# Kernel optimization log

Hardware: AMD Instinct MI355X
Metric: run time of the kernel (lower is better)

## Reference

```python
import jax, jax.numpy as jnp
import numpy as np
import jax.scipy.linalg as jsl

K = 4           # num_hops + 1
N = 4096        # nodes
D = 256         # in_dim == out_dim
S = 32          # subspace_dim
ETA = 0.5
EPS = 0.5


def setup_inputs() -> dict:
    key = jax.random.key(0)
    k1, k2, k3 = jax.random.split(key, 3)
    hops = jax.random.normal(k1, (K, N, D), dtype=jnp.float32)
    A = (jax.random.uniform(k2, (N, N)) < 0.01).astype(jnp.float32)
    A = jnp.maximum(A, A.T)
    A = jnp.fill_diagonal(A, 1.0, inplace=False)
    deg = A.sum(axis=1)
    L = jnp.diag(deg) - A  # graph Laplacian
    # orthonormal subspace bases via QR, as in __init__
    raw = jax.random.normal(k3, (K, D, S), dtype=jnp.float32)
    q, _ = jnp.linalg.qr(raw)
    U = q[:, :, :S]
    hop_weights = jnp.ones((K,), dtype=jnp.float32) / K
    threshold = jnp.full((D,), 0.05, dtype=jnp.float32)
    lambda_lap = jnp.asarray(0.1, dtype=jnp.float32)
    return {"hops": hops, "adj_mask": A, "L": L, "U": U,
            "hop_weights": hop_weights, "threshold": threshold,
            "lambda_lap": lambda_lap}


def reference(hops, adj_mask, L, U, hop_weights, threshold, lambda_lap):
    n = hops.shape[1]
    s = U.shape[-1]
    w = jax.nn.softmax(hop_weights, axis=0)
    mask_add = (1.0 - adj_mask) * -1e9  # [n, n]
    I_s = jnp.eye(s, dtype=hops.dtype)
    agg_total = jnp.zeros((hops.shape[2], n), dtype=hops.dtype)  # [d, n]
    coeff = s / (n * EPS ** 2)
    for k in range(K):  # small fixed hop count
        Uk = U[k]                      # [d, s]
        Zk = Uk.T @ hops[k].T          # [s, n]
        M_k = I_s + coeff * (Zk @ Zk.T)  # [s, s]
        cf = jsl.cho_factor(M_k)
        M_inv = jsl.cho_solve(cf, I_s)   # Cholesky inverse
        MZ = M_inv @ Zk                  # [s, n]
        scores = Zk.T @ MZ + mask_add    # [n, n] Mahalanobis-style attention
        alpha = jax.nn.softmax(scores, axis=1)
        grad_k = Uk @ (MZ @ alpha.T)     # [d, n]
        agg_total = agg_total + w[k] * grad_k
    H_agg = agg_total.T                  # [n, d]
    lap_grad = lambda_lap * (L @ H_agg)
    H_half = hops[0] + ETA * H_agg - ETA * lap_grad
    # soft-threshold (proximal step); in_dim == out_dim so no proj
    H_out = jnp.sign(H_half) * jax.nn.relu(jnp.abs(H_half) - threshold[None, :])
    # orthogonality regularizer over subspace bases
    orth_loss = jnp.asarray(0.0, dtype=hops.dtype)
    for k in range(K):
        UkTUk = U[k].T @ U[k]
        orth_loss = orth_loss + ((UkTUk - I_s) ** 2).sum()
        for l in range(k + 1, K):
            orth_loss = orth_loss + ((U[k].T @ U[l]) ** 2).sum()
    lap_smooth = jnp.sum(H_out * (L @ H_out))  # trace(H^T L H)
    return (H_out, orth_loss, lap_smooth, jax.lax.stop_gradient(w))
```

## Files before the change

kernel.cpp:

```cpp
#include <hip/hip_runtime.h>
#include <cstddef>

typedef unsigned short ushortt;
typedef unsigned int uintt;

static constexpr int Nn = 4096;
static constexpr int Dd = 256;
static constexpr int Ss = 32;
static constexpr int Kk = 4;
static constexpr int CAP = 160;
static constexpr float kEta   = 0.5f;
static constexpr float kCoeff = 0.03125f;

__device__ __forceinline__ float waveReduceSum(float v){
  #pragma unroll
  for (int off = 32; off > 0; off >>= 1) v += __shfl_down(v, off, 64);
  return v;
}
__device__ __forceinline__ float blo(uintt u){ return __uint_as_float(u << 16); }
__device__ __forceinline__ float bhi(uintt u){ return __uint_as_float(u & 0xffff0000u); }
__device__ __forceinline__ ushortt f2b(float x){
  uintt u = __float_as_uint(x);
  uintt r = (u + 0x7fffu + ((u >> 16) & 1u)) >> 16;
  return (ushortt)r;
}
__device__ __forceinline__ float b2f(ushortt u){ return __uint_as_float(((uintt)u) << 16); }

__global__ __launch_bounds__(256) void build_kernel(const float* __restrict__ A,
                                                    const float* __restrict__ hw,
                                                    int* __restrict__ deg,
                                                    int* __restrict__ colx,
                                                    float* __restrict__ out){
  int i = blockIdx.x, tid = threadIdx.x;
  if (i == 0 && tid == 0){
    out[1048576] = 0.f;
    out[1048577] = 0.f;
    float a0=hw[0], a1=hw[1], a2=hw[2], a3=hw[3];
    float mx = fmaxf(fmaxf(a0,a1), fmaxf(a2,a3));
    float e0=expf(a0-mx), e1=expf(a1-mx), e2=expf(a2-mx), e3=expf(a3-mx);
    float s = e0+e1+e2+e3;
    out[1048578]=e0/s; out[1048579]=e1/s; out[1048580]=e2/s; out[1048581]=e3/s;
  }
  int lane = tid & 63, w = tid >> 6;
  __shared__ int wbuf[4][96];
  __shared__ int wcnt[4];
  const float4* row4 = (const float4*)(A + (size_t)i * Nn);
  int cnt = 0;
  int base = w * 256;
  #pragma unroll
  for (int it = 0; it < 4; it++){
    int c4 = base + it * 64 + lane;
    float4 v = row4[c4];
    int f0 = (v.x != 0.f), f1 = (v.y != 0.f), f2 = (v.z != 0.f), f3 = (v.w != 0.f);
    int nf = f0 + f1 + f2 + f3;
    int pre = nf;
    #pragma unroll
    for (int off = 1; off < 64; off <<= 1){
      int o = __shfl_up(pre, off, 64);
      if (lane >= off) pre += o;
    }
    int tot = __shfl(pre, 63, 64);
    int pos = cnt + pre - nf;
    int j0 = c4 * 4;
    if (f0){ if (pos < 96) wbuf[w][pos] = j0;     pos++; }
    if (f1){ if (pos < 96) wbuf[w][pos] = j0 + 1; pos++; }
    if (f2){ if (pos < 96) wbuf[w][pos] = j0 + 2; pos++; }
    if (f3){ if (pos < 96) wbuf[w][pos] = j0 + 3; pos++; }
    cnt += tot;
  }
  if (cnt > 96) cnt = 96;
  if (lane == 0) wcnt[w] = cnt;
  __syncthreads();
  int off = 0;
  for (int ww = 0; ww < w; ww++) off += wcnt[ww];
  int total = wcnt[0] + wcnt[1] + wcnt[2] + wcnt[3];
  for (int idx = lane; idx < cnt; idx += 64){
    int p = off + idx;
    if (p < CAP) colx[(size_t)i * CAP + p] = wbuf[w][idx];
  }
  if (tid == 0) deg[i] = (total < CAP) ? total : CAP;
}

__global__ __launch_bounds__(256) void z_kernel(const float* __restrict__ hops,
                                                const float* __restrict__ U,
                                                float* __restrict__ Zt4){
  int b = blockIdx.x;
  int k = b >> 9;
  int i0 = (b & 511) * 8;
  __shared__ float Us[Ss][260];
  for (int t = threadIdx.x; t < Dd * Ss; t += 256){
    int s = t & 31, d = t >> 5;
    Us[s][d] = U[(size_t)k * Dd * Ss + t];
  }
  __syncthreads();
  int s = threadIdx.x & 31, ii = threadIdx.x >> 5;
  int i = i0 + ii;
  const float4* h4 = (const float4*)(hops + ((size_t)k * Nn + i) * Dd);
  const float4* u4 = (const float4*)(&Us[s][0]);
  float acc = 0.f;
  #pragma unroll 8
  for (int dq = 0; dq < 64; dq++){
    float4 h = h4[dq];
    float4 u = u4[dq];
    acc += h.x*u.x + h.y*u.y + h.z*u.z + h.w*u.w;
  }
  Zt4[(size_t)i * 128 + k * 32 + s] = acc;
}

__global__ __launch_bounds__(256) void mpart_kernel(const float* __restrict__ Zt4,
                                                    float* __restrict__ Mpart){
  int b = blockIdx.x;
  int k = b >> 4, ch = b & 15;
  int i0 = ch * 256;
  __shared__ float zs[256][33];
  for (int t = threadIdx.x; t < 256 * 32; t += 256){
    int ii = t >> 5, s = t & 31;
    zs[ii][s] = Zt4[(size_t)(i0 + ii) * 128 + k * 32 + s];
  }
  __syncthreads();
  int tid = threadIdx.x;
  int s2 = tid & 31, s1b = tid >> 5;
  float a0=0.f, a1=0.f, a2=0.f, a3=0.f;
  for (int ii = 0; ii < 256; ii++){
    float zc = zs[ii][s2];
    a0 = fmaf(zs[ii][s1b],      zc, a0);
    a1 = fmaf(zs[ii][8 + s1b],  zc, a1);
    a2 = fmaf(zs[ii][16 + s1b], zc, a2);
    a3 = fmaf(zs[ii][24 + s1b], zc, a3);
  }
  float* outp = Mpart + (size_t)b * 1024;
  outp[0 * 256 + tid] = a0;
  outp[1 * 256 + tid] = a1;
  outp[2 * 256 + tid] = a2;
  outp[3 * 256 + tid] = a3;
}

__global__ __launch_bounds__(256) void inv_kernel(const float* __restrict__ Mpart,
                                                  float* __restrict__ Minv){
  __shared__ float Msh[4][32][33];
  int tid = threadIdx.x;
  for (int e = tid; e < 4096; e += 256){
    int k = e >> 10, rc = e & 1023;
    float s = 0.f;
    for (int ch = 0; ch < 16; ch++) s += Mpart[(size_t)(k * 16 + ch) * 1024 + rc];
    int r = rc >> 5, c = rc & 31;
    Msh[k][r][c] = kCoeff * s + ((r == c) ? 1.f : 0.f);
  }
  __syncthreads();
  int k = tid >> 6, lane = tid & 63, r = lane & 31, half = lane >> 5;
  float a[32];
  #pragma unroll
  for (int j = 0; j < 32; j++) a[j] = half ? ((r == j) ? 1.f : 0.f) : Msh[k][r][j];
  #pragma unroll
  for (int p = 0; p < 32; p++){
    float app = __shfl(a[p], p, 64);
    float pinv = 1.f / app;
    float f = __shfl(a[p], r, 64);
    #pragma unroll
    for (int j = 0; j < 32; j++){
      float pr = __shfl(a[j], p + (half << 5), 64) * pinv;
      a[j] = (r == p) ? pr : fmaf(-f, pr, a[j]);
    }
  }
  if (half){
    #pragma unroll
    for (int j = 0; j < 32; j++) Minv[(size_t)k * 1024 + r * 32 + j] = a[j];
  }
}

__global__ __launch_bounds__(256) void mz_kernel(const float* __restrict__ Zt4,
                                                 const float* __restrict__ Minv,
                                                 ushortt* __restrict__ MZb){
  int b = blockIdx.x;
  int k = b >> 7;
  int i0 = (b & 127) * 32;
  __shared__ float mi[32][33];
  __shared__ float zs[32][33];
  for (int t = threadIdx.x; t < 1024; t += 256){
    int ii = t >> 5, s2 = t & 31;
    mi[ii][s2] = Minv[(size_t)k * 1024 + t];
    zs[ii][s2] = Zt4[(size_t)(i0 + ii) * 128 + k * 32 + s2];
  }
  __syncthreads();
  int s = threadIdx.x & 31;
  for (int rr = 0; rr < 4; rr++){
    int ii = rr * 8 + (threadIdx.x >> 5);
    float acc = 0.f;
    #pragma unroll
    for (int s2 = 0; s2 < 32; s2++) acc = fmaf(mi[s][s2], zs[ii][s2], acc);
    MZb[(size_t)(i0 + ii) * 128 + k * 32 + s] = f2b(acc);
  }
}

__global__ __launch_bounds__(256) void agg_kernel(const float* __restrict__ Zt4,
                                                  const ushortt* __restrict__ MZb,
                                                  const float* __restrict__ wvec,
                                                  const int* __restrict__ deg,
                                                  const int* __restrict__ colx,
                                                  float* __restrict__ Vw){
  int i = blockIdx.x, tid = threadIdx.x;
  int lane = tid & 63, k = tid >> 6;
  __shared__ int cols[CAP];
  __shared__ __align__(16) float zi[128];
  __shared__ float sc[4][CAP + 8];
  int m = deg[i];
  if (tid < 128) zi[tid] = Zt4[(size_t)i * 128 + tid];
  for (int t = tid; t < m; t += 256) cols[t] = colx[(size_t)i * CAP + t];
  __syncthreads();

  float zr[32];
  {
    const float4* z4 = (const float4*)(&zi[k * 32]);
    #pragma unroll
    for (int q = 0; q < 8; q++){
      float4 z = z4[q];
      zr[q*4+0]=z.x; zr[q*4+1]=z.y; zr[q*4+2]=z.z; zr[q*4+3]=z.w;
    }
  }
  float lmax = -3.0e38f;
  for (int t = lane; t < m; t += 64){
    int j = cols[t];
    const uint4* rp = (const uint4*)(MZb + ((size_t)j * 128 + k * 32));
    uint4 q0 = rp[0], q1 = rp[1], q2 = rp[2], q3 = rp[3];
    float acc = 0.f;
    acc += blo(q0.x)*zr[0] + bhi(q0.x)*zr[1] + blo(q0.y)*zr[2] + bhi(q0.y)*zr[3];
    acc += blo(q0.z)*zr[4] + bhi(q0.z)*zr[5] + blo(q0.w)*zr[6] + bhi(q0.w)*zr[7];
    acc += blo(q1.x)*zr[8] + bhi(q1.x)*zr[9] + blo(q1.y)*zr[10]+ bhi(q1.y)*zr[11];
    acc += blo(q1.z)*zr[12]+ bhi(q1.z)*zr[13]+ blo(q1.w)*zr[14]+ bhi(q1.w)*zr[15];
    acc += blo(q2.x)*zr[16]+ bhi(q2.x)*zr[17]+ blo(q2.y)*zr[18]+ bhi(q2.y)*zr[19];
    acc += blo(q2.z)*zr[20]+ bhi(q2.z)*zr[21]+ blo(q2.w)*zr[22]+ bhi(q2.w)*zr[23];
    acc += blo(q3.x)*zr[24]+ bhi(q3.x)*zr[25]+ blo(q3.y)*zr[26]+ bhi(q3.y)*zr[27];
    acc += blo(q3.z)*zr[28]+ bhi(q3.z)*zr[29]+ blo(q3.w)*zr[30]+ bhi(q3.w)*zr[31];
    sc[k][t] = acc;
    lmax = fmaxf(lmax, acc);
  }
  #pragma unroll
  for (int off = 32; off > 0; off >>= 1) lmax = fmaxf(lmax, __shfl_xor(lmax, off, 64));
  float lsum = 0.f;
  for (int t = lane; t < m; t += 64){
    float e = __expf(sc[k][t] - lmax);
    sc[k][t] = e;
    lsum += e;
  }
  #pragma unroll
  for (int off = 32; off > 0; off >>= 1) lsum += __shfl_xor(lsum, off, 64);
  float scale = wvec[k] / lsum;

  int c2 = lane & 15, h = lane >> 4;
  float a0 = 0.f, a1 = 0.f;
  #pragma unroll 4
  for (int t = h; t < m; t += 4){
    int j = cols[t];
    uintt u = *(const uintt*)(MZb + ((size_t)j * 128 + k * 32 + c2 * 2));
    float e = sc[k][t];
    a0 = fmaf(blo(u), e, a0);
    a1 = fmaf(bhi(u), e, a1);
  }
  a0 += __shfl_xor(a0, 16, 64); a0 += __shfl_xor(a0, 32, 64);
  a1 += __shfl_xor(a1, 16, 64); a1 += __shfl_xor(a1, 32, 64);
  if (h == 0){
    float2 v2 = make_float2(a0 * scale, a1 * scale);
    *(float2*)(Vw + (size_t)i * 128 + k * 32 + c2 * 2) = v2;
  }
}

__global__ __launch_bounds__(256) void gatherv_kernel(const float* __restrict__ Vw,
                                                      const float* __restrict__ lam_ptr,
                                                      const int* __restrict__ deg,
                                                      const int* __restrict__ colx,
                                                      float* __restrict__ cVc){
  int i = blockIdx.x, tid = threadIdx.x;
  int c = tid & 127, g = tid >> 7;
  __shared__ int cols[CAP];
  __shared__ float vred[2][128];
  int m = deg[i];
  for (int t = tid; t < m; t += 256) cols[t] = colx[(size_t)i * CAP + t];
  __syncthreads();
  float acc = 0.f;
  #pragma unroll 8
  for (int t = g; t < m; t += 2)
    acc += Vw[(size_t)cols[t] * 128 + c];
  vred[g][c] = acc;
  __syncthreads();
  if (tid < 128){
    float nb = vred[0][tid] + vred[1][tid];
    float lam = lam_ptr[0];
    float self = Vw[(size_t)i * 128 + tid];
    cVc[(size_t)i * 128 + tid] = kEta * (1.f - lam * (float)m) * self + kEta * lam * nb;
  }
}

__global__ __launch_bounds__(256) void transu_kernel(const float* __restrict__ U,
                                                     float* __restrict__ Ubt){
  int idx = blockIdx.x * 256 + threadIdx.x;
  int c = idx >> 8, d = idx & 255;
  int k = c >> 5, s = c & 31;
  Ubt[idx] = U[(size_t)k * Dd * Ss + (size_t)d * Ss + s];
}

__global__ __launch_bounds__(256) void houtblend_kernel(const float* __restrict__ cVc,
                                                        const float* __restrict__ Ubt,
                                                        const float* __restrict__ hops0,
                                                        const float* __restrict__ thr,
                                                        float* __restrict__ out,
                                                        ushortt* __restrict__ Hb){
  int i0 = blockIdx.x * 16;
  int tid = threadIdx.x;
  __shared__ float Cs[16][132];
  for (int t = tid; t < 16 * 128; t += 256){
    int ii = t >> 7, c = t & 127;
    Cs[ii][c] = cVc[(size_t)(i0 + ii) * 128 + c];
  }
  __syncthreads();
  int d4 = tid & 63, g = tid >> 6;
  float4 acc[4];
  #pragma unroll
  for (int r = 0; r < 4; r++) acc[r] = make_float4(0.f, 0.f, 0.f, 0.f);
  #pragma unroll 2
  for (int c = 0; c < 128; c++){
    float4 ub = ((const float4*)(Ubt + (size_t)c * 256))[d4];
    #pragma unroll
    for (int r = 0; r < 4; r++){
      float cs = Cs[g * 4 + r][c];
      acc[r].x = fmaf(cs, ub.x, acc[r].x);
      acc[r].y = fmaf(cs, ub.y, acc[r].y);
      acc[r].z = fmaf(cs, ub.z, acc[r].z);
      acc[r].w = fmaf(cs, ub.w, acc[r].w);
    }
  }
  float4 th = ((const float4*)thr)[d4];
  #pragma unroll
  for (int r = 0; r < 4; r++){
    int i = i0 + g * 4 + r;
    float4 hp = ((const float4*)(hops0 + (size_t)i * 256))[d4];
    float hx = hp.x + acc[r].x, hy = hp.y + acc[r].y;
    float hz = hp.z + acc[r].z, hw = hp.w + acc[r].w;
    float4 o;
    o.x = copysignf(fmaxf(fabsf(hx) - th.x, 0.f), hx);
    o.y = copysignf(fmaxf(fabsf(hy) - th.y, 0.f), hy);
    o.z = copysignf(fmaxf(fabsf(hz) - th.z, 0.f), hz);
    o.w = copysignf(fmaxf(fabsf(hw) - th.w, 0.f), hw);
    ((float4*)(out + (size_t)i * 256))[d4] = o;
    ushort4 hb;
    hb.x = f2b(o.x); hb.y = f2b(o.y); hb.z = f2b(o.z); hb.w = f2b(o.w);
    *((ushort4*)(Hb + (size_t)i * 256 + d4 * 4)) = hb;
  }
}

__global__ __launch_bounds__(256) void lap_kernel(const float* __restrict__ Hout,
                                                  const ushortt* __restrict__ Hb,
                                                  const int* __restrict__ deg,
                                                  const int* __restrict__ colx,
                                                  float* __restrict__ lap_part){
  int b = blockIdx.x;
  int i = b >> 1, half = b & 1;
  int tid = threadIdx.x;
  int dl = tid & 127, g = tid >> 7;
  int d = half * 128 + dl;
  __shared__ int cols[CAP];
  int m = deg[i];
  for (int t = tid; t < m; t += 256) cols[t] = colx[(size_t)i * CAP + t];
  __syncthreads();
  float nb = 0.f;
  #pragma unroll 8
  for (int t = g; t < m; t += 2)
    nb += b2f(Hb[(size_t)cols[t] * 256 + d]);
  float hi = Hout[(size_t)i * 256 + d];
  float part = -hi * nb;
  if (g == 0) part = fmaf((float)m * hi, hi, part);
  part = waveReduceSum(part);
  __shared__ float red[4];
  if ((tid & 63) == 0) red[tid >> 6] = part;
  __syncthreads();
  if (tid == 0) lap_part[b] = red[0] + red[1] + red[2] + red[3];
}

__global__ __launch_bounds__(256) void lapred_kernel(const float* __restrict__ lap_part,
                                                     float* __restrict__ out){
  int tid = threadIdx.x;
  float s = 0.f;
  const float4* p4 = (const float4*)lap_part;
  #pragma unroll
  for (int q = 0; q < 8; q++){
    float4 v = p4[q * 256 + tid];
    s += v.x + v.y + v.z + v.w;
  }
  s = waveReduceSum(s);
  __shared__ float red[4];
  if ((tid & 63) == 0) red[tid >> 6] = s;
  __syncthreads();
  if (tid == 0) out[1048577] = red[0] + red[1] + red[2] + red[3];
}

__global__ __launch_bounds__(256) void orth_kernel(const float* __restrict__ U,
                                                   float* __restrict__ orth_out){
  int g = blockIdx.x * 256 + threadIdx.x;
  int pair = g >> 10;
  int idx = g & 1023;
  int s1 = idx >> 5, s2 = idx & 31;
  const int pk_[10] = {0,0,0,0,1,1,1,2,2,3};
  const int pl_[10] = {0,1,2,3,1,2,3,2,3,3};
  int pk = pk_[pair], pl = pl_[pair];
  const float* Uk = U + (size_t)pk * Dd * Ss;
  const float* Ul = U + (size_t)pl * Dd * Ss;
  float dot = 0.f;
  for (int d = 0; d < Dd; d++) dot += Uk[d * Ss + s1] * Ul[d * Ss + s2];
  float val = dot - ((pk == pl && s1 == s2) ? 1.f : 0.f);
  val *= val;
  val = waveReduceSum(val);
  __shared__ float red[4];
  if ((threadIdx.x & 63) == 0) red[threadIdx.x >> 6] = val;
  __syncthreads();
  if (threadIdx.x == 0) atomicAdd(orth_out, red[0] + red[1] + red[2] + red[3]);
}

extern "C" void kernel_launch(void* const* d_in, const int* in_sizes, int n_in,
                              void* d_out, int out_size, void* d_ws, size_t ws_size,
                              hipStream_t stream)
{
  const float* hops = (const float*)d_in[0];
  const float* A    = (const float*)d_in[1];
  const float* L    = (const float*)d_in[2];
  const float* U    = (const float*)d_in[3];
  const float* hw   = (const float*)d_in[4];
  const float* thr  = (const float*)d_in[5];
  const float* lam  = (const float*)d_in[6];
  (void)L; (void)in_sizes; (void)n_in; (void)out_size; (void)ws_size;

  float* out = (float*)d_out;
  float* ws  = (float*)d_ws;

  float*   Zt4   = ws;
  float*   Vw    = ws + 524288;
  float*   cVc   = ws + 1048576;
  ushortt* MZb   = (ushortt*)(ws + 1572864);
  ushortt* Hb    = (ushortt*)(ws + 1835008);
  float*   Ubt   = ws + 2359296;
  float*   Mpart = ws + 2392064;
  float*   Minv  = ws + 2457600;
  int*     deg   = (int*)(ws + 2461696);
  int*     colx  = (int*)(ws + 2465792);
  float*   lapp  = ws + 3121152;

  float* orth_out = out + 1048576;
  float* w_out    = out + 1048578;

  build_kernel    <<<Nn, 256, 0, stream>>>(A, hw, deg, colx, out);
  transu_kernel   <<<128, 256, 0, stream>>>(U, Ubt);
  z_kernel        <<<Kk*512, 256, 0, stream>>>(hops, U, Zt4);
  mpart_kernel    <<<Kk*16, 256, 0, stream>>>(Zt4, Mpart);
  inv_kernel      <<<1, 256, 0, stream>>>(Mpart, Minv);
  mz_kernel       <<<Kk*128, 256, 0, stream>>>(Zt4, Minv, MZb);
  agg_kernel      <<<Nn, 256, 0, stream>>>(Zt4, MZb, w_out, deg, colx, Vw);
  gatherv_kernel  <<<Nn, 256, 0, stream>>>(Vw, lam, deg, colx, cVc);
  houtblend_kernel<<<256, 256, 0, stream>>>(cVc, Ubt, hops, thr, out, Hb);
  lap_kernel      <<<2*Nn, 256, 0, stream>>>(out, Hb, deg, colx, lapp);
  lapred_kernel   <<<1, 256, 0, stream>>>(lapp, out);
  orth_kernel     <<<40, 256, 0, stream>>>(U, orth_out);
}
```

Before: 317.8 us.

## Fuse neighbor gather into output blend and merge small kernels to cut launches

Folds the gatherv kernel into the output-blend kernel so each block gathers neighbor Vw rows itself and builds the blended coefficients in shared memory. This removes the cVc intermediate and one launch. The U transpose moves into z_kernel, the lap reduction becomes an extra block of orth_kernel, and agg_kernel's final gather now uses wider 8-byte loads with 4 accumulators. Together this drops three launches, but the fused kernel runs only 256 blocks for the gather work that previously used 4096 blocks, so occupancy and latency hiding may suffer.

New measurement: 329.6 us. +3.7%, slower.

```diff
diff --git a/kernel.cpp b/kernel.cpp
--- a/kernel.cpp
+++ b/kernel.cpp
@@ -83,7 +83,8 @@
 
 __global__ __launch_bounds__(256) void z_kernel(const float* __restrict__ hops,
                                                 const float* __restrict__ U,
-                                                float* __restrict__ Zt4){
+                                                float* __restrict__ Zt4,
+                                                float* __restrict__ Ubt){
   int b = blockIdx.x;
   int k = b >> 9;
   int i0 = (b & 511) * 8;
@@ -105,6 +106,12 @@
     acc += h.x*u.x + h.y*u.y + h.z*u.z + h.w*u.w;
   }
   Zt4[(size_t)i * 128 + k * 32 + s] = acc;
+  if (b < 128){
+    int idx = b * 256 + threadIdx.x;
+    int c = idx >> 8, d = idx & 255;
+    int kk = c >> 5, s2 = c & 31;
+    Ubt[idx] = U[(size_t)kk * Dd * Ss + (size_t)d * Ss + s2];
+  }
 }
 
 __global__ __launch_bounds__(256) void mpart_kernel(const float* __restrict__ Zt4,
@@ -246,70 +253,80 @@
   for (int off = 32; off > 0; off >>= 1) lsum += __shfl_xor(lsum, off, 64);
   float scale = wvec[k] / lsum;
 
-  int c2 = lane & 15, h = lane >> 4;
-  float a0 = 0.f, a1 = 0.f;
-  #pragma unroll 4
-  for (int t = h; t < m; t += 4){
+  int c8 = lane & 7, h = lane >> 3;
+  float a0 = 0.f, a1 = 0.f, a2 = 0.f, a3 = 0.f;
+  #pragma unroll 2
+  for (int t = h; t < m; t += 8){
     int j = cols[t];
-    uintt u = *(const uintt*)(MZb + ((size_t)j * 128 + k * 32 + c2 * 2));
+    uint2 u = *(const uint2*)(MZb + ((size_t)j * 128 + k * 32 + c8 * 4));
     float e = sc[k][t];
-    a0 = fmaf(blo(u), e, a0);
-    a1 = fmaf(bhi(u), e, a1);
-  }
-  a0 += __shfl_xor(a0, 16, 64); a0 += __shfl_xor(a0, 32, 64);
-  a1 += __shfl_xor(a1, 16, 64); a1 += __shfl_xor(a1, 32, 64);
+    a0 = fmaf(blo(u.x), e, a0);
+    a1 = fmaf(bhi(u.x), e, a1);
+    a2 = fmaf(blo(u.y), e, a2);
+    a3 = fmaf(bhi(u.y), e, a3);
+  }
+  #pragma unroll
+  for (int off = 8; off < 64; off <<= 1){
+    a0 += __shfl_xor(a0, off, 64);
+    a1 += __shfl_xor(a1, off, 64);
+    a2 += __shfl_xor(a2, off, 64);
+    a3 += __shfl_xor(a3, off, 64);
+  }
   if (h == 0){
-    float2 v2 = make_float2(a0 * scale, a1 * scale);
-    *(float2*)(Vw + (size_t)i * 128 + k * 32 + c2 * 2) = v2;
-  }
-}
-
-__global__ __launch_bounds__(256) void gatherv_kernel(const float* __restrict__ Vw,
-                                                      const float* __restrict__ lam_ptr,
-                                                      const int* __restrict__ deg,
-                                                      const int* __restrict__ colx,
-                                                      float* __restrict__ cVc){
-  int i = blockIdx.x, tid = threadIdx.x;
-  int c = tid & 127, g = tid >> 7;
-  __shared__ int cols[CAP];
-  __shared__ float vred[2][128];
-  int m = deg[i];
-  for (int t = tid; t < m; t += 256) cols[t] = colx[(size_t)i * CAP + t];
-  __syncthreads();
-  float acc = 0.f;
-  #pragma unroll 8
-  for (int t = g; t < m; t += 2)
-    acc += Vw[(size_t)cols[t] * 128 + c];
-  vred[g][c] = acc;
-  __syncthreads();
-  if (tid < 128){
-    float nb = vred[0][tid] + vred[1][tid];
-    float lam = lam_ptr[0];
-    float self = Vw[(size_t)i * 128 + tid];
-    cVc[(size_t)i * 128 + tid] = kEta * (1.f - lam * (float)m) * self + kEta * lam * nb;
-  }
-}
-
-__global__ __launch_bounds__(256) void transu_kernel(const float* __restrict__ U,
-                                                     float* __restrict__ Ubt){
-  int idx = blockIdx.x * 256 + threadIdx.x;
-  int c = idx >> 8, d = idx & 255;
-  int k = c >> 5, s = c & 31;
-  Ubt[idx] = U[(size_t)k * Dd * Ss + (size_t)d * Ss + s];
-}
-
-__global__ __launch_bounds__(256) void houtblend_kernel(const float* __restrict__ cVc,
+    float4 v4 = make_float4(a0 * scale, a1 * scale, a2 * scale, a3 * scale);
+    *(float4*)(Vw + (size_t)i * 128 + k * 32 + c8 * 4) = v4;
+  }
+}
+
+__global__ __launch_bounds__(256) void houtfused_kernel(const float* __restrict__ Vw,
                                                         const float* __restrict__ Ubt,
                                                         const float* __restrict__ hops0,
                                                         const float* __restrict__ thr,
+                                                        const float* __restrict__ lam_ptr,
+                                                        const int* __restrict__ deg,
+                                                        const int* __restrict__ colx,
                                                         float* __restrict__ out,
                                                         ushortt* __restrict__ Hb){
   int i0 = blockIdx.x * 16;
   int tid = threadIdx.x;
+  int lane = tid & 63, w = tid >> 6;
   __shared__ float Cs[16][132];
-  for (int t = tid; t < 16 * 128; t += 256){
-    int ii = t >> 7, c = t & 127;
-    Cs[ii][c] = cVc[(size_t)(i0 + ii) * 128 + c];
+  __shared__ int cols_s[16][CAP];
+  __shared__ int deg_s[16];
+  for (int rr = w; rr < 16; rr += 4){
+    int i = i0 + rr;
+    int m = deg[i];
+    if (lane == 0) deg_s[rr] = m;
+    for (int t = lane; t < m; t += 64) cols_s[rr][t] = colx[(size_t)i * CAP + t];
+  }
+  __syncthreads();
+  float lam = lam_ptr[0];
+  int nb2 = lane >> 5;
+  int c32 = lane & 31;
+  for (int rr = w; rr < 16; rr += 4){
+    int i = i0 + rr;
+    int m = deg_s[rr];
+    float4 acc = make_float4(0.f, 0.f, 0.f, 0.f);
+    for (int t = nb2; t < m; t += 2){
+      int j = cols_s[rr][t];
+      float4 v = ((const float4*)(Vw + (size_t)j * 128))[c32];
+      acc.x += v.x; acc.y += v.y; acc.z += v.z; acc.w += v.w;
+    }
+    acc.x += __shfl_xor(acc.x, 32, 64);
+    acc.y += __shfl_xor(acc.y, 32, 64);
+    acc.z += __shfl_xor(acc.z, 32, 64);
+    acc.w += __shfl_xor(acc.w, 32, 64);
+    if (nb2 == 0){
+      float4 self = ((const float4*)(Vw + (size_t)i * 128))[c32];
+      float ca = kEta * (1.f - lam * (float)m);
+      float cb = kEta * lam;
+      float4 o;
+      o.x = fmaf(ca, self.x, cb * acc.x);
+      o.y = fmaf(ca, self.y, cb * acc.y);
+      o.z = fmaf(ca, self.z, cb * acc.z);
+      o.w = fmaf(ca, self.w, cb * acc.w);
+      *(float4*)(&Cs[rr][c32 * 4]) = o;
+    }
   }
   __syncthreads();
   int d4 = tid & 63, g = tid >> 6;
@@ -375,26 +392,26 @@
   if (tid == 0) lap_part[b] = red[0] + red[1] + red[2] + red[3];
 }
 
-__global__ __launch_bounds__(256) void lapred_kernel(const float* __restrict__ lap_part,
-                                                     float* __restrict__ out){
+__global__ __launch_bounds__(256) void orth_kernel(const float* __restrict__ U,
+                                                   const float* __restrict__ lap_part,
+                                                   float* __restrict__ out){
   int tid = threadIdx.x;
-  float s = 0.f;
-  const float4* p4 = (const float4*)lap_part;
-  #pragma unroll
-  for (int q = 0; q < 8; q++){
-    float4 v = p4[q * 256 + tid];
-    s += v.x + v.y + v.z + v.w;
-  }
-  s = waveReduceSum(s);
-  __shared__ float red[4];
-  if ((tid & 63) == 0) red[tid >> 6] = s;
-  __syncthreads();
-  if (tid == 0) out[1048577] = red[0] + red[1] + red[2] + red[3];
-}
-
-__global__ __launch_bounds__(256) void orth_kernel(const float* __restrict__ U,
-                                                   float* __restrict__ orth_out){
-  int g = blockIdx.x * 256 + threadIdx.x;
+  if (blockIdx.x == 40){
+    float s = 0.f;
+    const float4* p4 = (const float4*)lap_part;
+    #pragma unroll
+    for (int q = 0; q < 8; q++){
+      float4 v = p4[q * 256 + tid];
+      s += v.x + v.y + v.z + v.w;
+    }
+    s = waveReduceSum(s);
+    __shared__ float redl[4];
+    if ((tid & 63) == 0) redl[tid >> 6] = s;
+    __syncthreads();
+    if (tid == 0) out[1048577] = redl[0] + redl[1] + redl[2] + redl[3];
+    return;
+  }
+  int g = blockIdx.x * 256 + tid;
   int pair = g >> 10;
   int idx = g & 1023;
   int s1 = idx >> 5, s2 = idx & 31;
@@ -409,9 +426,9 @@
   val *= val;
   val = waveReduceSum(val);
   __shared__ float red[4];
-  if ((threadIdx.x & 63) == 0) red[threadIdx.x >> 6] = val;
-  __syncthreads();
-  if (threadIdx.x == 0) atomicAdd(orth_out, red[0] + red[1] + red[2] + red[3]);
+  if ((tid & 63) == 0) red[tid >> 6] = val;
+  __syncthreads();
+  if (tid == 0) atomicAdd(out + 1048576, red[0] + red[1] + red[2] + red[3]);
 }
 
 extern "C" void kernel_launch(void* const* d_in, const int* in_sizes, int n_in,
@@ -432,7 +449,6 @@
 
   float*   Zt4   = ws;
   float*   Vw    = ws + 524288;
-  float*   cVc   = ws + 1048576;
   ushortt* MZb   = (ushortt*)(ws + 1572864);
   ushortt* Hb    = (ushortt*)(ws + 1835008);
   float*   Ubt   = ws + 2359296;
@@ -442,19 +458,15 @@
   int*     colx  = (int*)(ws + 2465792);
   float*   lapp  = ws + 3121152;
 
-  float* orth_out = out + 1048576;
-  float* w_out    = out + 1048578;
+  float* w_out = out + 1048578;
 
   build_kernel    <<<Nn, 256, 0, stream>>>(A, hw, deg, colx, out);
-  transu_kernel   <<<128, 256, 0, stream>>>(U, Ubt);
-  z_kernel        <<<Kk*512, 256, 0, stream>>>(hops, U, Zt4);
+  z_kernel        <<<Kk*512, 256, 0, stream>>>(hops, U, Zt4, Ubt);
   mpart_kernel    <<<Kk*16, 256, 0, stream>>>(Zt4, Mpart);
   inv_kernel      <<<1, 256, 0, stream>>>(Mpart, Minv);
   mz_kernel       <<<Kk*128, 256, 0, stream>>>(Zt4, Minv, MZb);
   agg_kernel      <<<Nn, 256, 0, stream>>>(Zt4, MZb, w_out, deg, colx, Vw);
-  gatherv_kernel  <<<Nn, 256, 0, stream>>>(Vw, lam, deg, colx, cVc);
-  houtblend_kernel<<<256, 256, 0, stream>>>(cVc, Ubt, hops, thr, out, Hb);
+  houtfused_kernel<<<256, 256, 0, stream>>>(Vw, Ubt, hops, thr, lam, deg, colx, out, Hb);
   lap_kernel      <<<2*Nn, 256, 0, stream>>>(out, Hb, deg, colx, lapp);
-  lapred_kernel   <<<1, 256, 0, stream>>>(lapp, out);
-  orth_kernel     <<<40, 256, 0, stream>>>(U, orth_out);
-}
+  orth_kernel     <<<41, 256, 0, stream>>>(U, lapp, out);
+}
```
